# Performance work log

Measured on AMD Instinct MI355X. Metric: run time of the kernel, lower is better.

The kernel has to match this reference:

```python
import jax, jax.numpy as jnp
import numpy as np

N = 8192
EMB = 256
NHID = 64
ALPHA = 0.2  # LeakyReLU negative slope
NEG_INF = -9e15


def setup_inputs() -> dict:
    key = jax.random.key(0)
    k1, k2, k3, k4 = jax.random.split(key, 4)
    inp = jax.random.normal(k1, (N, EMB), dtype=jnp.float32)
    adj = jax.random.randint(k2, (N, N), 0, 2, dtype=jnp.int32)
    W = jax.random.normal(k3, (EMB, NHID), dtype=jnp.float32) * 0.05
    a = jax.random.normal(k4, (2 * NHID,), dtype=jnp.float32) * 0.05
    return {"input": inp, "adj": adj, "W": W, "a": a}


def reference(input, adj, W, a):
    # h = W(input): [N, nhid]
    h = input @ W
    # e_ij = leakyrelu(h_i . a[:nhid] + h_j . a[nhid:])  (equiv. to concat-pairs @ a)
    s_src = h @ a[:NHID]   # [N]
    s_dst = h @ a[NHID:]   # [N]
    e = jax.nn.leaky_relu(s_src[:, None] + s_dst[None, :], ALPHA)  # [N, N]
    attention = jnp.where(adj > 0, e, NEG_INF)
    attention = jax.nn.softmax(attention, axis=1)
    # edge dropout p=0.0 (eval) -> identity
    h_prime = attention @ h  # [N, nhid]
    return h_prime
```

## Files before the change

kernel.cpp:

```cpp
#include <hip/hip_runtime.h>
#include <hip/hip_bf16.h>

#define N_NODES 8192
#define EMB 256
#define NHID 64
#define LOG2E 1.44269504088896340736f

typedef __attribute__((ext_vector_type(8))) short bf16x8;
typedef __attribute__((ext_vector_type(4))) float f32x4;

static __device__ __forceinline__ short f2bf(float f) {
  __hip_bfloat16 h = __float2bfloat16(f);
  return *reinterpret_cast<short*>(&h);
}

static __device__ __forceinline__ short f2bf_fast(float f) {
  unsigned u = __builtin_bit_cast(unsigned, f);
  return (short)((u + 0x8000u) >> 16);
}

__global__ __launch_bounds__(256) void gat_k1(
    const float* __restrict__ in, const float* __restrict__ W,
    const float* __restrict__ a, short* __restrict__ hT,
    float* __restrict__ ssrc, float* __restrict__ sdst) {
  int wave = threadIdx.x >> 6, lane = threadIdx.x & 63;
  int row = blockIdx.x * 4 + wave;
  int d = lane;
  const float4* in4 = reinterpret_cast<const float4*>(in + (size_t)row * EMB);
  float acc = 0.f;
#pragma unroll 4
  for (int k4 = 0; k4 < EMB / 4; ++k4) {
    float4 x = in4[k4];
    int k = k4 * 4;
    acc = fmaf(x.x, W[(k + 0) * NHID + d], acc);
    acc = fmaf(x.y, W[(k + 1) * NHID + d], acc);
    acc = fmaf(x.z, W[(k + 2) * NHID + d], acc);
    acc = fmaf(x.w, W[(k + 3) * NHID + d], acc);
  }
  hT[(size_t)d * N_NODES + row] = f2bf(acc);
  float p1 = acc * a[d];
  float p2 = acc * a[NHID + d];
#pragma unroll
  for (int off = 32; off > 0; off >>= 1) {
    p1 += __shfl_xor(p1, off);
    p2 += __shfl_xor(p2, off);
  }
  if (lane == 0) {
    ssrc[row] = p1 * LOG2E;
    sdst[row] = p2 * LOG2E;
  }
}

__global__ __launch_bounds__(256, 4) void gat_k2(
    const int* __restrict__ adj, const short* __restrict__ hT,
    const float* __restrict__ ssrc, const float* __restrict__ sdst,
    float* __restrict__ pacc, float* __restrict__ pz,
    int nsplit, int colsPer) {
  int rb = blockIdx.x / nsplit;
  int split = blockIdx.x % nsplit;
  int wv = threadIdx.x >> 6, lane = threadIdx.x & 63;
  int lrow = lane & 15, kg = lane >> 4;
  int r0 = rb * 64 + wv * 16;
  int row = r0 + lrow;
  float s_i = ssrc[row];
  const int* adjr = adj + (size_t)row * N_NODES;
  const short* hrow0 = hT + (size_t)(0 * 16 + lrow) * N_NODES;
  const short* hrow1 = hT + (size_t)(1 * 16 + lrow) * N_NODES;
  const short* hrow2 = hT + (size_t)(2 * 16 + lrow) * N_NODES;
  const short* hrow3 = hT + (size_t)(3 * 16 + lrow) * N_NODES;
  f32x4 acc0 = {0.f, 0.f, 0.f, 0.f};
  f32x4 acc1 = acc0, acc2 = acc0, acc3 = acc0;
  float zacc = 0.f;
  int jbase = split * colsPer + kg * 8;
  int nkt = colsPer >> 5;

  int4 aj0 = *reinterpret_cast<const int4*>(adjr + jbase);
  int4 aj1 = *reinterpret_cast<const int4*>(adjr + jbase + 4);
  float4 t0 = *reinterpret_cast<const float4*>(sdst + jbase);
  float4 t1 = *reinterpret_cast<const float4*>(sdst + jbase + 4);
  bf16x8 b0 = *reinterpret_cast<const bf16x8*>(hrow0 + jbase);
  bf16x8 b1 = *reinterpret_cast<const bf16x8*>(hrow1 + jbase);
  bf16x8 b2 = *reinterpret_cast<const bf16x8*>(hrow2 + jbase);
  bf16x8 b3 = *reinterpret_cast<const bf16x8*>(hrow3 + jbase);

  for (int kt = 0; kt < nkt; ++kt) {
    int jn = (kt + 1 < nkt) ? (jbase + (kt + 1) * 32) : jbase;
    int4 naj0 = *reinterpret_cast<const int4*>(adjr + jn);
    int4 naj1 = *reinterpret_cast<const int4*>(adjr + jn + 4);
    float4 nt0 = *reinterpret_cast<const float4*>(sdst + jn);
    float4 nt1 = *reinterpret_cast<const float4*>(sdst + jn + 4);
    bf16x8 nb0 = *reinterpret_cast<const bf16x8*>(hrow0 + jn);
    bf16x8 nb1 = *reinterpret_cast<const bf16x8*>(hrow1 + jn);
    bf16x8 nb2 = *reinterpret_cast<const bf16x8*>(hrow2 + jn);
    bf16x8 nb3 = *reinterpret_cast<const bf16x8*>(hrow3 + jn);

    float tv[8] = {t0.x, t0.y, t0.z, t0.w, t1.x, t1.y, t1.z, t1.w};
    int av[8] = {aj0.x, aj0.y, aj0.z, aj0.w, aj1.x, aj1.y, aj1.z, aj1.w};
    bf16x8 af;
#pragma unroll
    for (int e = 0; e < 8; ++e) {
      float x = s_i + tv[e];
      float lk = fmaxf(x, 0.2f * x);
      float ev = __builtin_amdgcn_exp2f(lk);
      float w = (av[e] != 0) ? ev : 0.f;
      zacc += w;
      af[e] = f2bf_fast(w);
    }
    acc0 = __builtin_amdgcn_mfma_f32_16x16x32_bf16(af, b0, acc0, 0, 0, 0);
    acc1 = __builtin_amdgcn_mfma_f32_16x16x32_bf16(af, b1, acc1, 0, 0, 0);
    acc2 = __builtin_amdgcn_mfma_f32_16x16x32_bf16(af, b2, acc2, 0, 0, 0);
    acc3 = __builtin_amdgcn_mfma_f32_16x16x32_bf16(af, b3, acc3, 0, 0, 0);

    aj0 = naj0; aj1 = naj1; t0 = nt0; t1 = nt1;
    b0 = nb0; b1 = nb1; b2 = nb2; b3 = nb3;
  }

  float z = zacc;
  z += __shfl_xor(z, 16);
  z += __shfl_xor(z, 32);
  if (lane < 16) pz[(size_t)split * N_NODES + r0 + lane] = z;

  float* pa = pacc + (size_t)split * (N_NODES * NHID);
#pragma unroll
  for (int reg = 0; reg < 4; ++reg) {
    int orow = r0 + kg * 4 + reg;
    pa[(size_t)orow * NHID + 0 * 16 + lrow] = acc0[reg];
    pa[(size_t)orow * NHID + 1 * 16 + lrow] = acc1[reg];
    pa[(size_t)orow * NHID + 2 * 16 + lrow] = acc2[reg];
    pa[(size_t)orow * NHID + 3 * 16 + lrow] = acc3[reg];
  }
}

__global__ __launch_bounds__(256) void gat_k3(
    const float* __restrict__ pacc, const float* __restrict__ pz,
    float* __restrict__ out, int nsplit) {
  int idx = blockIdx.x * 256 + threadIdx.x;
  int row = idx >> 6;
  float num = 0.f, den = 0.f;
  for (int s = 0; s < nsplit; ++s) {
    num += pacc[(size_t)s * (N_NODES * NHID) + idx];
    den += pz[(size_t)s * N_NODES + row];
  }
  out[idx] = num / den;
}

extern "C" void kernel_launch(void* const* d_in, const int* in_sizes, int n_in,
                              void* d_out, int out_size, void* d_ws, size_t ws_size,
                              hipStream_t stream) {
  (void)in_sizes; (void)n_in; (void)out_size;
  const float* in = (const float*)d_in[0];
  const int* adj = (const int*)d_in[1];
  const float* W = (const float*)d_in[2];
  const float* a = (const float*)d_in[3];
  float* out = (float*)d_out;

  int S = 8;
  while (S > 1 && (size_t)1114112 + (size_t)S * 2129920 > ws_size) S >>= 1;
  int colsPer = N_NODES / S;

  char* w = (char*)d_ws;
  short* hT = (short*)w;
  float* ssrc = (float*)(w + (1u << 20));
  float* sdst = ssrc + N_NODES;
  float* pz = sdst + N_NODES;
  float* pacc = pz + (size_t)S * N_NODES;

  gat_k1<<<N_NODES / 4, 256, 0, stream>>>(in, W, a, hT, ssrc, sdst);
  gat_k2<<<(N_NODES / 64) * S, 256, 0, stream>>>(adj, hT, ssrc, sdst, pacc, pz,
                                                 S, colsPer);
  gat_k3<<<(N_NODES * NHID) / 256, 256, 0, stream>>>(pacc, pz, out, S);
}
```

Measured before the change: 447.4 us.

## Pre-pack adjacency into a bitmask and read the mask in the attention kernel

A new pass, fused into the projection kernel's launch as extra blocks, streams the int32 adjacency matrix and packs it into one bit per edge. The attention/MFMA kernel then loads one 32-bit mask word per 32 columns instead of eight int32 values per lane per step. This is meant to cut the scattered, per-row strided adjacency traffic inside the compute-heavy kernel. The cost is an extra full coalesced read of the adjacency matrix plus an 8 MB mask write and reread. Workspace sizing grows to hold the mask.

```diff
diff --git a/kernel.cpp b/kernel.cpp
--- a/kernel.cpp
+++ b/kernel.cpp
@@ -5,6 +5,8 @@
 #define EMB 256
 #define NHID 64
 #define LOG2E 1.44269504088896340736f
+#define PACK_BLOCKS 2048
+#define K1_BLOCKS 2048
 
 typedef __attribute__((ext_vector_type(8))) short bf16x8;
 typedef __attribute__((ext_vector_type(4))) float f32x4;
@@ -19,12 +21,32 @@
   return (short)((u + 0x8000u) >> 16);
 }
 
-__global__ __launch_bounds__(256) void gat_k1(
+__global__ __launch_bounds__(256) void gat_k01(
+    const int* __restrict__ adj, unsigned* __restrict__ mask,
     const float* __restrict__ in, const float* __restrict__ W,
     const float* __restrict__ a, short* __restrict__ hT,
     float* __restrict__ ssrc, float* __restrict__ sdst) {
+  if (blockIdx.x < PACK_BLOCKS) {
+    const int nthreads = PACK_BLOCKS * 256;
+    const int nchunks = (N_NODES * N_NODES) / 32;
+    int tid = blockIdx.x * 256 + threadIdx.x;
+    for (int c = tid; c < nchunks; c += nthreads) {
+      const int4* p = reinterpret_cast<const int4*>(adj) + (size_t)c * 8;
+      unsigned m = 0;
+#pragma unroll
+      for (int j = 0; j < 8; ++j) {
+        int4 v = p[j];
+        m |= (unsigned)(v.x & 1) << (j * 4 + 0);
+        m |= (unsigned)(v.y & 1) << (j * 4 + 1);
+        m |= (unsigned)(v.z & 1) << (j * 4 + 2);
+        m |= (unsigned)(v.w & 1) << (j * 4 + 3);
+      }
+      mask[c] = m;
+    }
+    return;
+  }
   int wave = threadIdx.x >> 6, lane = threadIdx.x & 63;
-  int row = blockIdx.x * 4 + wave;
+  int row = (blockIdx.x - PACK_BLOCKS) * 4 + wave;
   int d = lane;
   const float4* in4 = reinterpret_cast<const float4*>(in + (size_t)row * EMB);
   float acc = 0.f;
@@ -52,7 +74,7 @@
 }
 
 __global__ __launch_bounds__(256, 4) void gat_k2(
-    const int* __restrict__ adj, const short* __restrict__ hT,
+    const unsigned* __restrict__ mask, const short* __restrict__ hT,
     const float* __restrict__ ssrc, const float* __restrict__ sdst,
     float* __restrict__ pacc, float* __restrict__ pz,
     int nsplit, int colsPer) {
@@ -63,7 +85,7 @@
   int r0 = rb * 64 + wv * 16;
   int row = r0 + lrow;
   float s_i = ssrc[row];
-  const int* adjr = adj + (size_t)row * N_NODES;
+  const unsigned* mrow = mask + (size_t)row * (N_NODES / 32) + split * (colsPer / 32);
   const short* hrow0 = hT + (size_t)(0 * 16 + lrow) * N_NODES;
   const short* hrow1 = hT + (size_t)(1 * 16 + lrow) * N_NODES;
   const short* hrow2 = hT + (size_t)(2 * 16 + lrow) * N_NODES;
@@ -73,9 +95,9 @@
   float zacc = 0.f;
   int jbase = split * colsPer + kg * 8;
   int nkt = colsPer >> 5;
+  int kgsh = kg * 8;
 
-  int4 aj0 = *reinterpret_cast<const int4*>(adjr + jbase);
-  int4 aj1 = *reinterpret_cast<const int4*>(adjr + jbase + 4);
+  unsigned mcur = mrow[0];
   float4 t0 = *reinterpret_cast<const float4*>(sdst + jbase);
   float4 t1 = *reinterpret_cast<const float4*>(sdst + jbase + 4);
   bf16x8 b0 = *reinterpret_cast<const bf16x8*>(hrow0 + jbase);
@@ -84,9 +106,9 @@
   bf16x8 b3 = *reinterpret_cast<const bf16x8*>(hrow3 + jbase);
 
   for (int kt = 0; kt < nkt; ++kt) {
-    int jn = (kt + 1 < nkt) ? (jbase + (kt + 1) * 32) : jbase;
-    int4 naj0 = *reinterpret_cast<const int4*>(adjr + jn);
-    int4 naj1 = *reinterpret_cast<const int4*>(adjr + jn + 4);
+    int ktn = (kt + 1 < nkt) ? kt + 1 : 0;
+    int jn = jbase + ktn * 32;
+    unsigned mnext = mrow[ktn];
     float4 nt0 = *reinterpret_cast<const float4*>(sdst + jn);
     float4 nt1 = *reinterpret_cast<const float4*>(sdst + jn + 4);
     bf16x8 nb0 = *reinterpret_cast<const bf16x8*>(hrow0 + jn);
@@ -95,14 +117,14 @@
     bf16x8 nb3 = *reinterpret_cast<const bf16x8*>(hrow3 + jn);
 
     float tv[8] = {t0.x, t0.y, t0.z, t0.w, t1.x, t1.y, t1.z, t1.w};
-    int av[8] = {aj0.x, aj0.y, aj0.z, aj0.w, aj1.x, aj1.y, aj1.z, aj1.w};
+    unsigned mb = (mcur >> kgsh) & 0xffu;
     bf16x8 af;
 #pragma unroll
     for (int e = 0; e < 8; ++e) {
       float x = s_i + tv[e];
       float lk = fmaxf(x, 0.2f * x);
       float ev = __builtin_amdgcn_exp2f(lk);
-      float w = (av[e] != 0) ? ev : 0.f;
+      float w = (mb & (1u << e)) ? ev : 0.f;
       zacc += w;
       af[e] = f2bf_fast(w);
     }
@@ -111,7 +133,7 @@
     acc2 = __builtin_amdgcn_mfma_f32_16x16x32_bf16(af, b2, acc2, 0, 0, 0);
     acc3 = __builtin_amdgcn_mfma_f32_16x16x32_bf16(af, b3, acc3, 0, 0, 0);
 
-    aj0 = naj0; aj1 = naj1; t0 = nt0; t1 = nt1;
+    mcur = mnext; t0 = nt0; t1 = nt1;
     b0 = nb0; b1 = nb1; b2 = nb2; b3 = nb3;
   }
 
@@ -155,7 +177,9 @@
   float* out = (float*)d_out;
 
   int S = 8;
-  while (S > 1 && (size_t)1114112 + (size_t)S * 2129920 > ws_size) S >>= 1;
+  while (S > 1 &&
+         (size_t)1114112 + (size_t)S * 2129920 + (size_t)8388608 > ws_size)
+    S >>= 1;
   int colsPer = N_NODES / S;
 
   char* w = (char*)d_ws;
@@ -164,9 +188,11 @@
   float* sdst = ssrc + N_NODES;
   float* pz = sdst + N_NODES;
   float* pacc = pz + (size_t)S * N_NODES;
+  unsigned* mask = (unsigned*)(pacc + (size_t)S * (N_NODES * NHID));
 
-  gat_k1<<<N_NODES / 4, 256, 0, stream>>>(in, W, a, hT, ssrc, sdst);
-  gat_k2<<<(N_NODES / 64) * S, 256, 0, stream>>>(adj, hT, ssrc, sdst, pacc, pz,
-                                                 S, colsPer);
+  gat_k01<<<PACK_BLOCKS + K1_BLOCKS, 256, 0, stream>>>(adj, mask, in, W, a, hT,
+                                                       ssrc, sdst);
+  gat_k2<<<(N_NODES / 64) * S, 256, 0, stream>>>(mask, hT, ssrc, sdst, pacc,
+                                                 pz, S, colsPer);
   gat_k3<<<(N_NODES * NHID) / 256, 256, 0, stream>>>(pacc, pz, out, S);
 }
```

Result: slower. 487.6 us (+9.0%).
